# Kernel tuning notes

Measured on AMD Instinct MI355X. Metric: run time of the kernel, lower is better.

The kernel has to match this reference:

```python
import jax, jax.numpy as jnp
import numpy as np

K = 3
KK = K * K


def conv3x3(x, w, b):
    # x: [B,C,H,W], w: [O,C,3,3]
    y = jax.lax.conv_general_dilated(x, w, (1, 1), ((1, 1), (1, 1)),
                                     dimension_numbers=('NCHW', 'OIHW', 'NCHW'))
    return y + b[None, :, None, None]


def deform_conv(x, offset, w, b):
    # torchvision.ops.deform_conv2d, 3x3, pad=1, stride=1, no mask.
    B, C, H, W = x.shape
    off = offset.reshape(B, KK, 2, H, W)  # per kernel tap: (dy, dx)
    ky = jnp.repeat(jnp.arange(K, dtype=x.dtype) - 1, K)  # [9]
    kx = jnp.tile(jnp.arange(K, dtype=x.dtype) - 1, K)
    py = jnp.arange(H, dtype=x.dtype)[None, None, :, None] + ky[None, :, None, None] + off[:, :, 0]
    px = jnp.arange(W, dtype=x.dtype)[None, None, None, :] + kx[None, :, None, None] + off[:, :, 1]
    y0 = jnp.floor(py)
    x0 = jnp.floor(px)
    wy = (py - y0)[:, None]  # [B,1,9,H,W]
    wx = (px - x0)[:, None]
    y0i = y0.astype(jnp.int32)
    x0i = x0.astype(jnp.int32)
    xf = x.reshape(B, C, H * W)

    def corner(yi, xi):
        valid = ((yi >= 0) & (yi < H) & (xi >= 0) & (xi < W))
        idx = jnp.clip(yi, 0, H - 1) * W + jnp.clip(xi, 0, W - 1)  # [B,9,H,W]
        g = jax.vmap(lambda xb, ib: xb[:, ib.reshape(-1)])(xf, idx)  # [B,C,9*H*W]
        return g.reshape(B, C, KK, H, W) * valid[:, None].astype(x.dtype)

    val = (corner(y0i, x0i) * (1 - wy) * (1 - wx)
           + corner(y0i, x0i + 1) * (1 - wy) * wx
           + corner(y0i + 1, x0i) * wy * (1 - wx)
           + corner(y0i + 1, x0i + 1) * wy * wx)  # [B,C,9,H,W]
    out = jnp.einsum('bckhw,ock->bohw', val, w.reshape(w.shape[0], C, KK))
    return out + b[None, :, None, None]


def se_gate(x, w1, b1, w2, b2):
    # global avg pool -> 1x1 conv -> relu -> 1x1 conv -> sigmoid -> scale
    m = x.mean((2, 3))  # [B,C]
    h = jax.nn.relu(jnp.einsum('bc,rc->br', m, w1) + b1)
    g = jax.nn.sigmoid(jnp.einsum('br,cr->bc', h, w2) + b2)
    return x * g[:, :, None, None]


def resize_bilinear(x, oh, ow):
    # F.interpolate(mode='bilinear', align_corners=False)
    B, C, H, W = x.shape

    def coords(n_in, n_out):
        src = (jnp.arange(n_out, dtype=x.dtype) + 0.5) * (n_in / n_out) - 0.5
        src = jnp.clip(src, 0.0, n_in - 1)
        i0 = jnp.floor(src).astype(jnp.int32)
        i1 = jnp.minimum(i0 + 1, n_in - 1)
        return i0, i1, (src - i0).astype(x.dtype)

    y0, y1, wy = coords(H, oh)
    x = x[:, :, y0, :] * (1 - wy)[None, None, :, None] + x[:, :, y1, :] * wy[None, None, :, None]
    c0, c1, wc = coords(W, ow)
    x = x[:, :, :, c0] * (1 - wc)[None, None, None, :] + x[:, :, :, c1] * wc[None, None, None, :]
    return x


def setup_inputs() -> dict:
    key = jax.random.key(0)
    ks = jax.random.split(key, 12)
    B, C, H, W = 4, 64, 128, 128
    L, O, R = 4, 64, 4  # levels, out_channels, reduction=64//16
    d = {
        'x': jax.random.normal(ks[0], (B, C, H, W), jnp.float32),
        'off_w': jax.random.normal(ks[1], (L, 2 * KK, C, 3, 3), jnp.float32) * 0.01,
        'off_b': jax.random.normal(ks[2], (L, 2 * KK), jnp.float32) * 0.01,
        'dc_w': jax.random.normal(ks[3], (L, O, C, 3, 3), jnp.float32) * 0.05,
        'dc_b': jax.random.normal(ks[4], (L, O), jnp.float32) * 0.05,
        'se_w1': jax.random.normal(ks[5], (L, R, O), jnp.float32) * 0.1,
        'se_b1': jax.random.normal(ks[6], (L, R), jnp.float32) * 0.1,
        'se_w2': jax.random.normal(ks[7], (L, O, R), jnp.float32) * 0.1,
        'se_b2': jax.random.normal(ks[8], (L, O), jnp.float32) * 0.1,
        'fuse_w': jax.random.normal(ks[9], (O, L * O), jnp.float32) * 0.05,
        'fuse_b': jax.random.normal(ks[10], (O,), jnp.float32) * 0.05,
    }
    return d


def reference(x, off_w, off_b, dc_w, dc_b, se_w1, se_b1, se_w2, se_b2, fuse_w, fuse_b):
    B, _, H, W = x.shape
    L = off_w.shape[0]
    cur = x
    feats = []
    for i in range(L):
        if i > 0:
            cur = resize_bilinear(cur, cur.shape[2] // 2, cur.shape[3] // 2)
        off = conv3x3(cur, off_w[i], off_b[i])
        cur = deform_conv(cur, off, dc_w[i], dc_b[i])
        cur = se_gate(cur, se_w1[i], se_b1[i], se_w2[i], se_b2[i])
        feats.append(resize_bilinear(cur, H, W))
    for i in range(L - 2, -1, -1):
        feats[i] = feats[i] + feats[i + 1]
    fused = jnp.concatenate(feats, axis=1)  # [B, L*O, H, W]
    return jnp.einsum('bchw,oc->bohw', fused, fuse_w) + fuse_b[None, :, None, None]
```

## Files before the change

kernel.cpp:

```cpp
#include <hip/hip_runtime.h>
#include <hip/hip_bf16.h>
#include <math.h>


constexpr int Bn = 4;

typedef __attribute__((ext_vector_type(8))) short short8;
typedef __attribute__((ext_vector_type(4))) float f32x4;
typedef __attribute__((ext_vector_type(4))) unsigned uint4v;

static __device__ __forceinline__ short f2b(float f){
  union { float f; unsigned u; } v; v.f = f;
  unsigned r = v.u + 0x7fffu + ((v.u >> 16) & 1u);
  return (short)(r >> 16);
}
static __device__ __forceinline__ unsigned f2b2(float x, float y){
  union { __hip_bfloat162 h; unsigned u; } cv;
  cv.h = __float22bfloat162_rn(make_float2(x, y));
  return cv.u;
}
static __device__ __forceinline__ float blo(unsigned u){ return __uint_as_float(u << 16); }
static __device__ __forceinline__ float bhi(unsigned u){ return __uint_as_float(u & 0xffff0000u); }

constexpr size_t OFF_CUR   = 0;
constexpr size_t OFF_DC    = OFF_CUR  + 4194304;
constexpr size_t OFF_T0    = OFF_DC   + 4194304;
constexpr size_t OFF_T1    = OFF_T0   + 4194304;
constexpr size_t OFF_T2    = OFF_T1   + 1048576;
constexpr size_t OFF_T3    = OFF_T2   + 262144;
constexpr size_t OFF_WSUMT = OFF_T3   + 65536;
constexpr size_t OFF_DCWT  = OFF_WSUMT + 8192;
constexpr size_t OFF_OWT   = OFF_DCWT  + 73728;
constexpr size_t OFF_SUMS  = OFF_OWT   + 36864;

__global__ void prep_k(const float* __restrict__ dc_w, const float* __restrict__ off_w,
                       const float* __restrict__ fuse_w, float* __restrict__ ws){
  int i = blockIdx.x * 256 + threadIdx.x;
  short* dcwT  = (short*)(ws + OFF_DCWT);
  short* owT   = (short*)(ws + OFF_OWT);
  short* wsumT = (short*)(ws + OFF_WSUMT);
  if (i < 147456){
    int oc = i / 576, r = i % 576, k = r >> 6, c = r & 63;
    dcwT[i] = f2b(dc_w[(oc*64 + c)*9 + k]);
  } else if (i < 147456 + 73728){
    int t = i - 147456;
    int lm = t / 576, l = lm >> 5, m = lm & 31, r = t % 576, k = r >> 6, c = r & 63;
    owT[t] = (m < 18) ? f2b(off_w[((l*18 + m)*64 + c)*9 + k]) : (short)0;
  } else if (i < 147456 + 73728 + 16384){
    int t = i - (147456 + 73728);
    int l = t / 4096, r = t % 4096, o = r / 64, c = r % 64;
    float s = 0.f;
    for (int jl = 0; jl <= l; jl++) s += fuse_w[o*256 + jl*64 + c];
    wsumT[t] = f2b(s);
  } else if (i < 147456 + 73728 + 16384 + 65536){
    ws[OFF_SUMS + (i - (147456 + 73728 + 16384))] = 0.f;
  }
}

__global__ __launch_bounds__(256) void cvt_k(const float* __restrict__ x, unsigned* __restrict__ cur){
  __shared__ float t[64][65];
  int tile = blockIdx.x;
  int b = tile >> 8, p0 = (tile & 255) << 6;
  int tx = threadIdx.x & 63, ty = threadIdx.x >> 6;
  #pragma unroll
  for (int c = ty; c < 64; c += 4)
    t[c][tx] = x[(((size_t)(b << 6) + c) << 14) + p0 + tx];
  __syncthreads();
  int u = threadIdx.x & 31, pr = threadIdx.x >> 5;
  #pragma unroll
  for (int i = 0; i < 8; i++){
    int pp = pr + i*8;
    unsigned v = f2b2(t[2*u][pp], t[2*u + 1][pp]);
    cur[((size_t)(b << 14) + p0 + pp)*32 + u] = v;
  }
}

template<int H, int LVL>
__global__ __launch_bounds__(256, 6) void deform_k(
    const unsigned* __restrict__ cur, const float* __restrict__ ws_all,
    const float* __restrict__ off_bias, const float* __restrict__ dc_bias,
    float* __restrict__ dc, float* __restrict__ sums){
  constexpr int W = H, P = H * W;
  constexpr int PITCHB = 584 * 2;
  constexpr int TPR = W/4, TPB = P/16;
  __shared__ __align__(16) short valA[16][584];
  __shared__ float offsP[2][16][18];
  __shared__ float4 tapW[144];
  __shared__ int4   tapI[144];
  const short* owt = (const short*)(ws_all + OFF_OWT) + LVL * 32 * 576;
  const short* dcw = (const short*)(ws_all + OFF_DCWT) + (size_t)LVL * 64 * 576;
  const int tid = threadIdx.x;
  const int wave = tid >> 6, lane = tid & 63;
  const int c0 = lane & 15, quad = lane >> 4, q4 = quad * 4;
  const int half = lane >> 5, cc = lane & 31;
  const int b = blockIdx.x / TPB;
  const int rr = blockIdx.x % TPB;
  const int hrow = (rr / TPR) * 4, wcol = (rr % TPR) * 4;
  const char* curc = (const char*)(cur + (size_t)b * P * 32) + cc * 4;
  char* valc = (char*)valA + wave * (4 * PITCHB);

  #pragma unroll
  for (int i = 0; i < 18; i++){
    const int t0 = 2*i, t1 = t0 + 1;
    const int p0l = t0/9, k0 = t0%9, p1l = t1/9, k1 = t1%9;
    int yy0 = hrow + wave + k0/3 - 1, xx0 = wcol + p0l + k0%3 - 1;
    int yy1 = hrow + wave + k1/3 - 1, xx1 = wcol + p1l + k1%3 - 1;
    bool v0 = ((unsigned)yy0 < (unsigned)H) & ((unsigned)xx0 < (unsigned)W);
    bool v1 = ((unsigned)yy1 < (unsigned)H) & ((unsigned)xx1 < (unsigned)W);
    int  i0 = v0 ? (yy0*W + xx0) : 0,  i1 = v1 ? (yy1*W + xx1) : 0;
    int   idx = half ? i1 : i0;
    bool  vv  = half ? v1 : v0;
    unsigned uv = *(const unsigned*)(curc + (size_t)idx * 128);
    uv = vv ? uv : 0u;
    const int ob0 = p0l*PITCHB + k0*128, ob1 = p1l*PITCHB + k1*128;
    *(unsigned*)(valc + (half ? ob1 : ob0) + cc*4) = uv;
  }
  __syncthreads();

  {
    const int colw = wave & 1, kh = wave >> 1;
    f32x4 oacc = {0,0,0,0};
    #pragma unroll
    for (int kb = 0; kb < 9; kb++){
      int kk = kh*9 + kb;
      short8 a  = *(const short8*)&valA[c0][kk*32 + quad*8];
      short8 bf = *(const short8*)&owt[(colw*16 + c0)*576 + kk*32 + quad*8];
      oacc = __builtin_amdgcn_mfma_f32_16x16x32_bf16(a, bf, oacc, 0, 0, 0);
    }
    int comp = colw*16 + c0;
    if (comp < 18){
      #pragma unroll
      for (int r = 0; r < 4; r++) offsP[kh][q4 + r][comp] = oacc[r];
    }
  }
  __syncthreads();

  if (tid < 144){
    int p = tid / 9, k = tid % 9;
    int h = hrow + (p >> 2), w = wcol + (p & 3);
    float oy = offsP[0][p][2*k]     + offsP[1][p][2*k]     + off_bias[LVL*18 + 2*k];
    float ox = offsP[0][p][2*k + 1] + offsP[1][p][2*k + 1] + off_bias[LVL*18 + 2*k + 1];
    float py = (float)(h + k/3 - 1) + oy;
    float px = (float)(w + k%3 - 1) + ox;
    float y0f = floorf(py), x0f = floorf(px);
    float fy = py - y0f, fx = px - x0f;
    int y0 = (int)y0f, x0 = (int)x0f, y1 = y0 + 1, x1 = x0 + 1;
    bool vy0 = (y0 >= 0) & (y0 < H), vy1 = (y1 >= 0) & (y1 < H);
    bool vx0 = (x0 >= 0) & (x0 < W), vx1 = (x1 >= 0) & (x1 < W);
    int y0c = min(max(y0, 0), H-1), y1c = min(max(y1, 0), H-1);
    int x0c = min(max(x0, 0), W-1), x1c = min(max(x1, 0), W-1);
    float gy = 1.f - fy, gx = 1.f - fx;
    tapW[tid] = make_float4((vy0 & vx0) ? gy*gx : 0.f,
                            (vy0 & vx1) ? gy*fx : 0.f,
                            (vy1 & vx0) ? fy*gx : 0.f,
                            (vy1 & vx1) ? fy*fx : 0.f);
    tapI[tid] = make_int4((y0c*W + x0c) << 7, (y0c*W + x1c) << 7,
                          (y1c*W + x0c) << 7, (y1c*W + x1c) << 7);
  }
  __syncthreads();

  #pragma unroll
  for (int i = 0; i < 18; i++){
    int T = wave*36 + 2*i + half;
    float4 wv = tapW[T];
    int4   ti = tapI[T];
    unsigned u0 = *(const unsigned*)(curc + ti.x);
    unsigned u1 = *(const unsigned*)(curc + ti.y);
    unsigned u2 = *(const unsigned*)(curc + ti.z);
    unsigned u3 = *(const unsigned*)(curc + ti.w);
    float vx = wv.x*blo(u0) + wv.y*blo(u1) + wv.z*blo(u2) + wv.w*blo(u3);
    float vy = wv.x*bhi(u0) + wv.y*bhi(u1) + wv.z*bhi(u2) + wv.w*bhi(u3);
    unsigned pk = f2b2(vx, vy);
    const int t0 = 2*i, t1 = t0 + 1;
    const int ob0 = (t0/9)*PITCHB + (t0%9)*128, ob1 = (t1/9)*PITCHB + (t1%9)*128;
    *(unsigned*)(valc + (half ? ob1 : ob0) + cc*4) = pk;
  }
  __syncthreads();

  const int n = wave*16 + c0;
  float bt2 = dc_bias[LVL*64 + n];
  f32x4 d0 = {bt2, bt2, bt2, bt2}, d1 = {0,0,0,0};
  #pragma unroll
  for (int kb = 0; kb < 9; kb++){
    short8 a  = *(const short8*)&valA[c0][kb*32 + quad*8];
    short8 bf = *(const short8*)&dcw[n*576 + kb*32 + quad*8];
    d0 = __builtin_amdgcn_mfma_f32_16x16x32_bf16(a, bf, d0, 0, 0, 0);
  }
  #pragma unroll
  for (int kb = 9; kb < 18; kb++){
    short8 a  = *(const short8*)&valA[c0][kb*32 + quad*8];
    short8 bf = *(const short8*)&dcw[n*576 + kb*32 + quad*8];
    d1 = __builtin_amdgcn_mfma_f32_16x16x32_bf16(a, bf, d1, 0, 0, 0);
  }
  f32x4 acc;
  #pragma unroll
  for (int r = 0; r < 4; r++) acc[r] = d0[r] + d1[r];
  float* dcb = dc + ((size_t)b*P + (size_t)(hrow + quad)*W + wcol)*64;
  #pragma unroll
  for (int r = 0; r < 4; r++) dcb[r*64 + n] = acc[r];
  float s = acc[0] + acc[1] + acc[2] + acc[3];
  s += __shfl_xor(s, 16);
  s += __shfl_xor(s, 32);
  if (quad == 0) atomicAdd(&sums[(LVL*16 + (blockIdx.x & 15))*256 + (b << 6) + n], s);
}

template<int W, int LVL>
__global__ __launch_bounds__(256) void fuse_gd_k(
    const float* __restrict__ dcv, const float* __restrict__ sums,
    const float* __restrict__ se_w1, const float* __restrict__ se_b1,
    const float* __restrict__ se_w2, const float* __restrict__ se_b2,
    const float* __restrict__ ws_all, float* __restrict__ tmp, unsigned* __restrict__ curn){
  constexpr int P = W * W;
  constexpr bool POOL = (LVL < 3);
  constexpr float invP = 1.f / (float)P;
  __shared__ __align__(16) float fS[64][68];
  __shared__ __align__(16) float gsh[64];
  const short* wsl = (const short*)(ws_all + OFF_WSUMT) + LVL * 4096;
  const int tid = threadIdx.x, wave = tid >> 6, lane = tid & 63;
  const int c0 = lane & 15, quad = lane >> 4, q4 = quad * 4;
  int b, rp = 0, cs = 0;
  if (POOL){
    constexpr int tilesPerB = P / 64, tilesPerRow = W / 32;
    b = blockIdx.x / tilesPerB;
    int r = blockIdx.x % tilesPerB;
    rp = r / tilesPerRow; cs = r % tilesPerRow;
  } else {
    b = (blockIdx.x * 64) / P;
  }

  {
    int sg = tid >> 6, c = tid & 63;
    float part = 0.f;
    #pragma unroll
    for (int s = 0; s < 4; s++) part += sums[(LVL*16 + sg*4 + s)*256 + (b << 6) + c];
    fS[sg][c] = part;
    __syncthreads();
    if (tid < 64){
      int r = tid & 3, j = tid >> 2;
      float hp = 0.f;
      #pragma unroll
      for (int q = 0; q < 4; q++){
        int cq = j*4 + q;
        float m = (fS[0][cq] + fS[1][cq] + fS[2][cq] + fS[3][cq]) * invP;
        hp += m * se_w1[(LVL*4 + r)*64 + cq];
      }
      hp += __shfl_xor(hp, 4);  hp += __shfl_xor(hp, 8);
      hp += __shfl_xor(hp, 16); hp += __shfl_xor(hp, 32);
      float hr = fmaxf(hp + se_b1[LVL*4 + r], 0.f);
      float a = se_b2[LVL*64 + tid];
      #pragma unroll
      for (int r2 = 0; r2 < 4; r2++)
        a += __shfl(hr, r2) * se_w2[(LVL*64 + tid)*4 + r2];
      gsh[tid] = 1.f / (1.f + expf(-a));
    }
    __syncthreads();
  }

  float4 g4 = *(const float4*)&gsh[c0*4];
  #pragma unroll
  for (int i = 0; i < 4; i++){
    int lp = wave*16 + (lane >> 4) + i*4;
    size_t gpix = POOL ? ((size_t)b*P + (size_t)(2*rp + (lp >> 5))*W + cs*32 + (lp & 31))
                       : ((size_t)blockIdx.x*64 + lp);
    float4 d = *(const float4*)&dcv[gpix*64 + c0*4];
    float4 v = make_float4(d.x*g4.x, d.y*g4.y, d.z*g4.z, d.w*g4.w);
    *(float4*)&fS[lp][c0*4] = v;
  }
  __syncthreads();
  f32x4 acc[4] = {{0,0,0,0},{0,0,0,0},{0,0,0,0},{0,0,0,0}};
  #pragma unroll
  for (int kb = 0; kb < 2; kb++){
    float4 lo = *(const float4*)&fS[wave*16 + c0][kb*32 + quad*8];
    float4 hi = *(const float4*)&fS[wave*16 + c0][kb*32 + quad*8 + 4];
    uint4v ua = {f2b2(lo.x, lo.y), f2b2(lo.z, lo.w), f2b2(hi.x, hi.y), f2b2(hi.z, hi.w)};
    short8 a = __builtin_bit_cast(short8, ua);
    #pragma unroll
    for (int t = 0; t < 4; t++){
      short8 bf = *(const short8*)&wsl[(t*16 + c0)*64 + kb*32 + quad*8];
      acc[t] = __builtin_amdgcn_mfma_f32_16x16x32_bf16(a, bf, acc[t], 0, 0, 0);
    }
  }
  #pragma unroll
  for (int t = 0; t < 4; t++){
    int n = t*16 + c0;
    size_t plane = ((size_t)(b << 6) + n) * P;
    size_t pix = POOL ? ((size_t)(2*rp + (wave >> 1))*W + cs*32 + (wave & 1)*16 + q4)
                      : ((size_t)(blockIdx.x*64) - (size_t)b*P + wave*16 + q4);
    *(f32x4*)&tmp[plane + pix] = acc[t];
  }
  if constexpr (POOL){
    int j = tid >> 4, uu = tid & 15;
    float4 p0 = *(const float4*)&fS[2*j][uu*4];
    float4 p1 = *(const float4*)&fS[2*j + 1][uu*4];
    float4 p2 = *(const float4*)&fS[32 + 2*j][uu*4];
    float4 p3 = *(const float4*)&fS[33 + 2*j][uu*4];
    float4 av = make_float4(0.25f*(p0.x + p1.x + p2.x + p3.x),
                            0.25f*(p0.y + p1.y + p2.y + p3.y),
                            0.25f*(p0.z + p1.z + p2.z + p3.z),
                            0.25f*(p0.w + p1.w + p2.w + p3.w));
    uint2 pv = make_uint2(f2b2(av.x, av.y), f2b2(av.z, av.w));
    *(uint2*)&curn[((size_t)b*(P/4) + (size_t)rp*(W/2) + cs*16 + j)*32 + uu*2] = pv;
  }
}

__global__ void final_k(const float* __restrict__ ws_all, const float* __restrict__ fuse_bias,
                        float* __restrict__ out){
  int i = blockIdx.x * 256 + threadIdx.x;
  int w = i & 127, h = (i >> 7) & 127, o = (i >> 14) & 63, b = i >> 20;
  float acc = fuse_bias[o] + ws_all[OFF_T0 + (((size_t)(b << 6) + o) << 14) + (h << 7) + w];
  const float* tarr[3] = {ws_all + OFF_T1, ws_all + OFF_T2, ws_all + OFF_T3};
  #pragma unroll
  for (int li = 0; li < 3; li++){
    int l = li + 1, Hl = 128 >> l;
    float scale = 1.0f / (float)(1 << l);
    float sy = fminf(fmaxf((h + 0.5f)*scale - 0.5f, 0.f), (float)(Hl - 1));
    float sx = fminf(fmaxf((w + 0.5f)*scale - 0.5f, 0.f), (float)(Hl - 1));
    int y0 = (int)sy, x0 = (int)sx;
    float fy = sy - y0, fx = sx - x0;
    int y1 = min(y0 + 1, Hl - 1), x1 = min(x0 + 1, Hl - 1);
    const float* tb = tarr[li] + (size_t)((b << 6) + o) * Hl * Hl;
    float v00 = tb[y0*Hl + x0], v01 = tb[y0*Hl + x1];
    float v10 = tb[y1*Hl + x0], v11 = tb[y1*Hl + x1];
    acc += (1.f-fy)*((1.f-fx)*v00 + fx*v01) + fy*((1.f-fx)*v10 + fx*v11);
  }
  out[i] = acc;
}

extern "C" void kernel_launch(void* const* d_in, const int* in_sizes, int n_in,
                              void* d_out, int out_size, void* d_ws, size_t ws_size,
                              hipStream_t stream){
  (void)in_sizes; (void)n_in; (void)out_size; (void)ws_size;
  const float* x      = (const float*)d_in[0];
  const float* off_w  = (const float*)d_in[1];
  const float* off_b  = (const float*)d_in[2];
  const float* dc_w   = (const float*)d_in[3];
  const float* dc_b   = (const float*)d_in[4];
  const float* se_w1  = (const float*)d_in[5];
  const float* se_b1  = (const float*)d_in[6];
  const float* se_w2  = (const float*)d_in[7];
  const float* se_b2  = (const float*)d_in[8];
  const float* fuse_w = (const float*)d_in[9];
  const float* fuse_b = (const float*)d_in[10];
  float* out = (float*)d_out;
  float* ws = (float*)d_ws;
  unsigned* cur = (unsigned*)(ws + OFF_CUR);
  float* dc   = ws + OFF_DC;
  float* tmp[4] = {ws + OFF_T0, ws + OFF_T1, ws + OFF_T2, ws + OFF_T3};
  float* sums = ws + OFF_SUMS;

  prep_k<<<(303104 + 255)/256, 256, 0, stream>>>(dc_w, off_w, fuse_w, ws);
  cvt_k<<<1024, 256, 0, stream>>>(x, cur);

  deform_k<128,0><<<4096, 256, 0, stream>>>(cur, ws, off_b, dc_b, dc, sums);
  fuse_gd_k<128,0><<<1024, 256, 0, stream>>>(dc, sums, se_w1, se_b1, se_w2, se_b2, ws, tmp[0], cur);
  deform_k<64,1><<<1024, 256, 0, stream>>>(cur, ws, off_b, dc_b, dc, sums);
  fuse_gd_k<64,1><<<256, 256, 0, stream>>>(dc, sums, se_w1, se_b1, se_w2, se_b2, ws, tmp[1], cur);
  deform_k<32,2><<<256, 256, 0, stream>>>(cur, ws, off_b, dc_b, dc, sums);
  fuse_gd_k<32,2><<<64, 256, 0, stream>>>(dc, sums, se_w1, se_b1, se_w2, se_b2, ws, tmp[2], cur);
  deform_k<16,3><<<64, 256, 0, stream>>>(cur, ws, off_b, dc_b, dc, sums);
  fuse_gd_k<16,3><<<16, 256, 0, stream>>>(dc, sums, se_w1, se_b1, se_w2, se_b2, ws, tmp[3], nullptr);

  final_k<<<16384, 256, 0, stream>>>(ws, fuse_b, out);
}
```

Measured before the change: 235.2 us.

## Load shared 6x6 halo patch for offset conv and widen deform gathers

The offset-conv im2col, which gathered 9 taps per pixel from global memory, is replaced by a single 6x6 halo patch load into shared memory. The offset MFMA reads its A fragments directly from that patch, and offsP is aliased into spare space in valA. The bilinear gather now has each lane handle 4 channels with 8-byte loads, and tap indices are stored as 16-bit values. Launch bounds rise to 7 blocks per CU, trading register headroom for occupancy and relying on 16-bit pixel indices.

After: 238.7 us. Within noise of the previous version (+1.5%).

```diff
diff --git a/kernel.cpp b/kernel.cpp
--- a/kernel.cpp
+++ b/kernel.cpp
@@ -8,6 +8,7 @@
 typedef __attribute__((ext_vector_type(8))) short short8;
 typedef __attribute__((ext_vector_type(4))) float f32x4;
 typedef __attribute__((ext_vector_type(4))) unsigned uint4v;
+typedef __attribute__((ext_vector_type(4))) unsigned short ushort4v;
 
 static __device__ __forceinline__ short f2b(float f){
   union { float f; unsigned u; } v; v.f = f;
@@ -76,7 +77,7 @@
 }
 
 template<int H, int LVL>
-__global__ __launch_bounds__(256, 6) void deform_k(
+__global__ __launch_bounds__(256, 7) void deform_k(
     const unsigned* __restrict__ cur, const float* __restrict__ ws_all,
     const float* __restrict__ off_bias, const float* __restrict__ dc_bias,
     float* __restrict__ dc, float* __restrict__ sums){
@@ -84,53 +85,63 @@
   constexpr int PITCHB = 584 * 2;
   constexpr int TPR = W/4, TPB = P/16;
   __shared__ __align__(16) short valA[16][584];
-  __shared__ float offsP[2][16][18];
-  __shared__ float4 tapW[144];
-  __shared__ int4   tapI[144];
+  __shared__ __align__(16) float4 tapW[144];
+  __shared__ __align__(8)  unsigned short tapIs[144][4];
+  short* patch = &valA[0][0];
+  float* offsP = (float*)((char*)&valA[0][0] + 8192);
   const short* owt = (const short*)(ws_all + OFF_OWT) + LVL * 32 * 576;
   const short* dcw = (const short*)(ws_all + OFF_DCWT) + (size_t)LVL * 64 * 576;
   const int tid = threadIdx.x;
   const int wave = tid >> 6, lane = tid & 63;
   const int c0 = lane & 15, quad = lane >> 4, q4 = quad * 4;
-  const int half = lane >> 5, cc = lane & 31;
   const int b = blockIdx.x / TPB;
   const int rr = blockIdx.x % TPB;
   const int hrow = (rr / TPR) * 4, wcol = (rr % TPR) * 4;
-  const char* curc = (const char*)(cur + (size_t)b * P * 32) + cc * 4;
-  char* valc = (char*)valA + wave * (4 * PITCHB);
-
-  #pragma unroll
-  for (int i = 0; i < 18; i++){
-    const int t0 = 2*i, t1 = t0 + 1;
-    const int p0l = t0/9, k0 = t0%9, p1l = t1/9, k1 = t1%9;
-    int yy0 = hrow + wave + k0/3 - 1, xx0 = wcol + p0l + k0%3 - 1;
-    int yy1 = hrow + wave + k1/3 - 1, xx1 = wcol + p1l + k1%3 - 1;
-    bool v0 = ((unsigned)yy0 < (unsigned)H) & ((unsigned)xx0 < (unsigned)W);
-    bool v1 = ((unsigned)yy1 < (unsigned)H) & ((unsigned)xx1 < (unsigned)W);
-    int  i0 = v0 ? (yy0*W + xx0) : 0,  i1 = v1 ? (yy1*W + xx1) : 0;
-    int   idx = half ? i1 : i0;
-    bool  vv  = half ? v1 : v0;
-    unsigned uv = *(const unsigned*)(curc + (size_t)idx * 128);
-    uv = vv ? uv : 0u;
-    const int ob0 = p0l*PITCHB + k0*128, ob1 = p1l*PITCHB + k1*128;
-    *(unsigned*)(valc + (half ? ob1 : ob0) + cc*4) = uv;
+  const unsigned* curu = cur + (size_t)b * P * 32;
+
+  {
+    #pragma unroll
+    for (int i = 0; i < 3; i++){
+      if (i < 2 || quad == 0){
+        int p36 = wave*9 + i*4 + quad;
+        int r6 = p36 / 6, c6 = p36 - r6*6;
+        int yy = hrow - 1 + r6, xx = wcol - 1 + c6;
+        bool v = ((unsigned)yy < (unsigned)H) & ((unsigned)xx < (unsigned)W);
+        int idx = v ? (yy*W + xx) : 0;
+        uint2 d = *(const uint2*)(curu + (size_t)idx*32 + c0*2);
+        if (!v){ d.x = 0u; d.y = 0u; }
+        *(uint2*)(patch + p36*72 + c0*4) = d;
+      }
+    }
   }
   __syncthreads();
 
   {
     const int colw = wave & 1, kh = wave >> 1;
+    const char* pb = (const char*)patch + ((c0 >> 2) * 6 + (c0 & 3)) * 144 + quad * 16;
+    const short* wrow = owt + (colw*16 + c0)*576 + quad*8;
     f32x4 oacc = {0,0,0,0};
-    #pragma unroll
-    for (int kb = 0; kb < 9; kb++){
-      int kk = kh*9 + kb;
-      short8 a  = *(const short8*)&valA[c0][kk*32 + quad*8];
-      short8 bf = *(const short8*)&owt[(colw*16 + c0)*576 + kk*32 + quad*8];
-      oacc = __builtin_amdgcn_mfma_f32_16x16x32_bf16(a, bf, oacc, 0, 0, 0);
+    if (kh == 0){
+      #pragma unroll
+      for (int kb = 0; kb < 9; kb++){
+        const int tap = kb >> 1;
+        short8 a  = *(const short8*)(pb + ((tap/3)*864 + (tap%3)*144 + (kb&1)*64));
+        short8 bf = *(const short8*)&wrow[kb*32];
+        oacc = __builtin_amdgcn_mfma_f32_16x16x32_bf16(a, bf, oacc, 0, 0, 0);
+      }
+    } else {
+      #pragma unroll
+      for (int kb = 0; kb < 9; kb++){
+        const int kk = 9 + kb, tap = kk >> 1;
+        short8 a  = *(const short8*)(pb + ((tap/3)*864 + (tap%3)*144 + (kk&1)*64));
+        short8 bf = *(const short8*)&wrow[kk*32];
+        oacc = __builtin_amdgcn_mfma_f32_16x16x32_bf16(a, bf, oacc, 0, 0, 0);
+      }
     }
     int comp = colw*16 + c0;
     if (comp < 18){
       #pragma unroll
-      for (int r = 0; r < 4; r++) offsP[kh][q4 + r][comp] = oacc[r];
+      for (int r = 0; r < 4; r++) offsP[kh*288 + (q4 + r)*18 + comp] = oacc[r];
     }
   }
   __syncthreads();
@@ -138,8 +149,8 @@
   if (tid < 144){
     int p = tid / 9, k = tid % 9;
     int h = hrow + (p >> 2), w = wcol + (p & 3);
-    float oy = offsP[0][p][2*k]     + offsP[1][p][2*k]     + off_bias[LVL*18 + 2*k];
-    float ox = offsP[0][p][2*k + 1] + offsP[1][p][2*k + 1] + off_bias[LVL*18 + 2*k + 1];
+    float oy = offsP[p*18 + 2*k]     + offsP[288 + p*18 + 2*k]     + off_bias[LVL*18 + 2*k];
+    float ox = offsP[p*18 + 2*k + 1] + offsP[288 + p*18 + 2*k + 1] + off_bias[LVL*18 + 2*k + 1];
     float py = (float)(h + k/3 - 1) + oy;
     float px = (float)(w + k%3 - 1) + ox;
     float y0f = floorf(py), x0f = floorf(px);
@@ -154,26 +165,32 @@
                             (vy0 & vx1) ? gy*fx : 0.f,
                             (vy1 & vx0) ? fy*gx : 0.f,
                             (vy1 & vx1) ? fy*fx : 0.f);
-    tapI[tid] = make_int4((y0c*W + x0c) << 7, (y0c*W + x1c) << 7,
-                          (y1c*W + x0c) << 7, (y1c*W + x1c) << 7);
-  }
-  __syncthreads();
-
-  #pragma unroll
-  for (int i = 0; i < 18; i++){
-    int T = wave*36 + 2*i + half;
-    float4 wv = tapW[T];
-    int4   ti = tapI[T];
-    unsigned u0 = *(const unsigned*)(curc + ti.x);
-    unsigned u1 = *(const unsigned*)(curc + ti.y);
-    unsigned u2 = *(const unsigned*)(curc + ti.z);
-    unsigned u3 = *(const unsigned*)(curc + ti.w);
-    float vx = wv.x*blo(u0) + wv.y*blo(u1) + wv.z*blo(u2) + wv.w*blo(u3);
-    float vy = wv.x*bhi(u0) + wv.y*bhi(u1) + wv.z*bhi(u2) + wv.w*bhi(u3);
-    unsigned pk = f2b2(vx, vy);
-    const int t0 = 2*i, t1 = t0 + 1;
-    const int ob0 = (t0/9)*PITCHB + (t0%9)*128, ob1 = (t1/9)*PITCHB + (t1%9)*128;
-    *(unsigned*)(valc + (half ? ob1 : ob0) + cc*4) = pk;
+    ushort4v ti = { (unsigned short)(y0c*W + x0c), (unsigned short)(y0c*W + x1c),
+                    (unsigned short)(y1c*W + x0c), (unsigned short)(y1c*W + x1c) };
+    *(ushort4v*)tapIs[tid] = ti;
+  }
+  __syncthreads();
+
+  {
+    const char* curc8 = (const char*)curu + c0*8;
+    int T = wave*36 + quad;
+    int p = T/9, k = T - p*9;
+    #pragma unroll
+    for (int i = 0; i < 9; i++){
+      float4 wv = tapW[T];
+      uint2 tw = *(const uint2*)tapIs[T];
+      uint2 u0 = *(const uint2*)(curc8 + ((tw.x & 0xffffu) << 7));
+      uint2 u1 = *(const uint2*)(curc8 + ((tw.x >> 16) << 7));
+      uint2 u2 = *(const uint2*)(curc8 + ((tw.y & 0xffffu) << 7));
+      uint2 u3 = *(const uint2*)(curc8 + ((tw.y >> 16) << 7));
+      float a0 = wv.x*blo(u0.x) + wv.y*blo(u1.x) + wv.z*blo(u2.x) + wv.w*blo(u3.x);
+      float a1 = wv.x*bhi(u0.x) + wv.y*bhi(u1.x) + wv.z*bhi(u2.x) + wv.w*bhi(u3.x);
+      float a2 = wv.x*blo(u0.y) + wv.y*blo(u1.y) + wv.z*blo(u2.y) + wv.w*blo(u3.y);
+      float a3 = wv.x*bhi(u0.y) + wv.y*bhi(u1.y) + wv.z*bhi(u2.y) + wv.w*bhi(u3.y);
+      uint2 pk; pk.x = f2b2(a0, a1); pk.y = f2b2(a2, a3);
+      *(uint2*)((char*)&valA[0][0] + p*PITCHB + k*128 + c0*8) = pk;
+      T += 4; k += 4; if (k >= 9){ k -= 9; ++p; }
+    }
   }
   __syncthreads();
 
```
